# Kernel optimization log

Measured on AMD Instinct MI355X. Metric: run time of the kernel, lower is better.

## Reference

```python
import jax, jax.numpy as jnp
import numpy as np
import math

INPUT_FRAMES = 12
FUTURE_FRAMES = 26
T_STEPS = INPUT_FRAMES + FUTURE_FRAMES - 1  # 37
HD = 64   # hidden_dim
D = 16    # d_attn
CIN = 3   # input channels (time='stable')
COUT = 2  # output_dim
H, W = 24, 48


def conv2d(x, w, b, pad):
    # x: (N,C,H,W), w: (O,I,kh,kw)
    y = jax.lax.conv_general_dilated(x, w, (1, 1), [(pad, pad), (pad, pad)],
                                     dimension_numbers=('NCHW', 'OIHW', 'NCHW'))
    return y + b[None, :, None, None]


def spatial_attn(q, k, v):
    # q,k,v: (N,C,S); attention over spatial dim S
    scale = 1.0 / math.sqrt(q.shape[1])
    scores = jnp.einsum('ncs,nct->nst', q, k) * scale  # (N,S,S)
    a = jax.nn.softmax(scores, axis=-1)
    return jnp.einsum('nst,nct->ncs', a, v)


def setup_inputs() -> dict:
    key = jax.random.key(0)
    ks = jax.random.split(key, 8)
    s = 0.05
    inp = {
        'input_x': jax.random.normal(ks[0], (16, T_STEPS, H, W, CIN), dtype=jnp.float32),
        # ConvLSTM gate conv: in = CIN+HD, out = 4*HD, 3x3
        'conv_w': jax.random.normal(ks[1], (4 * HD, CIN + HD, 3, 3), dtype=jnp.float32) * s,
        'conv_b': jnp.zeros((4 * HD,), jnp.float32),
        # SA memory module
        'h_w': jax.random.normal(ks[2], (3 * D, HD, 1, 1), dtype=jnp.float32) * s,
        'h_b': jnp.zeros((3 * D,), jnp.float32),
        'm_w': jax.random.normal(ks[3], (2 * D, HD, 1, 1), dtype=jnp.float32) * s,
        'm_b': jnp.zeros((2 * D,), jnp.float32),
        'z_w': jax.random.normal(ks[4], (D, 2 * D, 1, 1), dtype=jnp.float32) * s,
        'z_b': jnp.zeros((D,), jnp.float32),
        'o_w': jax.random.normal(ks[5], (3 * HD, HD + D, 3, 3), dtype=jnp.float32) * s,
        'o_b': jnp.zeros((3 * HD,), jnp.float32),
        # final 1x1 projection to output_dim
        'out_w': jax.random.normal(ks[6], (COUT, HD, 1, 1), dtype=jnp.float32) * s,
        'out_b': jnp.zeros((COUT,), jnp.float32),
    }
    return inp


def reference(input_x, conv_w, conv_b, h_w, h_b, m_w, m_b, z_w, z_b, o_w, o_b, out_w, out_b):
    x = jnp.transpose(input_x, (0, 1, 4, 2, 3))  # (N,T,C,H,W)
    N = x.shape[0]
    S = H * W

    h0 = jnp.zeros((N, HD, H, W), x.dtype)
    carry0 = (h0, h0, h0, jnp.zeros((N, COUT, H, W), x.dtype))

    def step(carry, inp_t):
        h, c, m, prev_out = carry
        xt, t = inp_t  # xt: (N,CIN,H,W), t: scalar
        autoreg = jnp.concatenate([prev_out, xt[:, 2:]], axis=1)
        feed = jnp.where(t < INPUT_FRAMES, xt, autoreg)
        # ConvLSTM gates
        comb = conv2d(jnp.concatenate([feed, h], axis=1), conv_w, conv_b, 1)
        ci, cf, co, cg = jnp.split(comb, 4, axis=1)
        i = jax.nn.sigmoid(ci)
        f = jax.nn.sigmoid(cf)
        o = jax.nn.sigmoid(co)
        g = jnp.tanh(cg)
        c = f * c + i * g
        h = o * jnp.tanh(c)
        # self-attention memory
        hq, hk, hv = jnp.split(conv2d(h, h_w, h_b, 0), 3, axis=1)
        mk, mv = jnp.split(conv2d(m, m_w, m_b, 0), 2, axis=1)
        Zh = spatial_attn(hq.reshape(N, D, S), hk.reshape(N, D, S), hv.reshape(N, D, S))
        Zm = spatial_attn(hq.reshape(N, D, S), mk.reshape(N, D, S), mv.reshape(N, D, S))
        Z = conv2d(jnp.concatenate([Zh.reshape(N, D, H, W), Zm.reshape(N, D, H, W)], axis=1), z_w, z_b, 0)
        iog = conv2d(jnp.concatenate([Z, h], axis=1), o_w, o_b, 1)
        si, sg, so = jnp.split(iog, 3, axis=1)
        si = jax.nn.sigmoid(si)
        sg = jnp.tanh(sg)
        m = si * sg + (1.0 - si) * m
        h = jax.nn.sigmoid(so) * m
        out = conv2d(h, out_w, out_b, 0)
        return (h, c, m, out), out

    xs = (jnp.transpose(x, (1, 0, 2, 3, 4)), jnp.arange(T_STEPS))
    _, outs = jax.lax.scan(step, carry0, xs)
    outputs = jnp.transpose(outs, (1, 0, 2, 3, 4))  # (N,T,COUT,H,W)

    nino = outputs[:, -FUTURE_FRAMES:, 0, 10:13, 19:30].mean(axis=(2, 3))  # (N,26)
    nino_pred = (nino[:, :-2] + nino[:, 1:-1] + nino[:, 2:]) / 3.0          # (N,24)
    return outputs, nino_pred
```

## Files before the change

kernel.cpp:

```cpp
#include <hip/hip_runtime.h>
#include <math.h>

#define HD 64
#define DATT 16
#define NCIN 3
#define NCOUT 2
#define HH 24
#define WW 48
#define SS (HH*WW)
#define NB 16
#define TSTEPS 37
#define INPUT_FRAMES 12

#define PR 26
#define PC 52
#define PHW (PR*PC)

#define OFF_H     0
#define OFF_C     1384448
#define OFF_M     2564096
#define OFF_FEED  3743744
#define OFF_Z     3808640
#define ZERO_END  4154752
#define OFF_QKV   4154752
#define OFF_MKV   5039488
#define OFF_HB    5629312
#define OFF_IOG   8873344
#define OFF_BF2   12412288
#define OFF_BF    12596864

typedef __attribute__((ext_vector_type(8))) short short8;
typedef __attribute__((ext_vector_type(4))) float f32x4;

__device__ __forceinline__ float sigmoidf_(float x) {
    return 1.0f / (1.0f + __expf(-x));
}
__device__ __forceinline__ unsigned short f2bf(float f) {
    unsigned u = __float_as_uint(f);
    unsigned r = (u + 0x7fffu + ((u >> 16) & 1u)) >> 16;
    return (unsigned short)r;
}
__device__ __forceinline__ float bf2f(unsigned short b) {
    return __uint_as_float(((unsigned)b) << 16);
}
__device__ __forceinline__ unsigned packbf(float f) {
    unsigned short hi = f2bf(f);
    unsigned short lo = f2bf(f - bf2f(hi));
    return ((unsigned)lo << 16) | (unsigned)hi;
}
__device__ __forceinline__ float unpackbf(unsigned pk) {
    return __uint_as_float(pk << 16) + __uint_as_float(pk & 0xffff0000u);
}
__device__ __forceinline__ unsigned cvt_pk_bf16(float a, float b) {
    unsigned r;
    asm("v_cvt_pk_bf16_f32 %0, %1, %2" : "=v"(r) : "v"(a), "v"(b));
    return r;
}
__device__ __forceinline__ int permrow(int t) {
    int kb = t >> 5, tl = t & 31;
    int quad = tl >> 3, rr = tl & 7;
    return kb * 32 + ((rr >= 4) ? 16 : 0) + quad * 4 + (rr & 3);
}

__global__ void k_zero(float* __restrict__ p, int n4) {
    int i = blockIdx.x * blockDim.x + threadIdx.x;
    if (i < n4) ((float4*)p)[i] = make_float4(0.f, 0.f, 0.f, 0.f);
}

__global__ void k_prep_bf2(const float* __restrict__ cw, unsigned short* __restrict__ bbuf) {
    int idx = blockIdx.x * 256 + threadIdx.x;
    if (idx >= 344064) return;
    int j    = idx & 7;
    int lane = (idx >> 3) & 63;
    int ki   = (idx >> 9) % 21;
    int nt   = (idx / 10752) % 16;
    int p    = idx / 172032;
    int k = ki * 32 + (lane >> 4) * 8 + j;
    int ncol = nt * 16 + (lane & 15);
    unsigned short v = 0;
    if (k < 648) {
        int c = k % 72, kt = k / 72;
        if (c < 67) {
            float w = cw[ncol * 603 + c * 9 + kt];
            unsigned short hi = f2bf(w);
            v = (p == 0) ? hi : f2bf(w - bf2f(hi));
        }
    }
    bbuf[idx] = v;
}

__global__ void k_prep_bf(const float* __restrict__ ow, unsigned short* __restrict__ bbuf) {
    int idx = blockIdx.x * 256 + threadIdx.x;
    if (idx >= 282624) return;
    int j    = idx & 7;
    int lane = (idx >> 3) & 63;
    int ki   = (idx >> 9) % 23;
    int nt   = (idx / 11776) % 12;
    int p    = idx / 141312;
    int k = ki * 32 + (lane >> 4) * 8 + j;
    int ncol = nt * 16 + (lane & 15);
    unsigned short v = 0;
    if (k < 720) {
        int c = k % 80, kt = k / 80;
        float w = ow[ncol * 720 + c * 9 + kt];
        unsigned short hi = f2bf(w);
        v = (p == 0) ? hi : f2bf(w - bf2f(hi));
    }
    bbuf[idx] = v;
}

__global__ void k_feed0(const float* __restrict__ x, unsigned* __restrict__ feed) {
    int i = blockIdx.x * blockDim.x + threadIdx.x;
    if (i >= NB * 3 * SS) return;
    int s = i % SS;
    int ch = (i / SS) % 3;
    int n = i / (3 * SS);
    int y = s / WW, xx = s % WW;
    float v = x[(((size_t)(n * TSTEPS + 0) * HH + y) * WW + xx) * NCIN + ch];
    feed[((size_t)(n * 3 + ch) * PR + (y + 1)) * PC + (xx + 1)] = packbf(v);
}

#define ZOFF2 (3*52*73)
__global__ __launch_bounds__(256) void k_conv_lstm_mfma(
    const unsigned* __restrict__ feed, const unsigned* __restrict__ hin,
    const unsigned short* __restrict__ bbuf, const float* __restrict__ cb,
    float* __restrict__ c, unsigned* __restrict__ hout)
{
    __shared__ int lds[3 * 52 * 73 + 8];
    const int y0 = blockIdx.x;
    const int nb = blockIdx.y;
    const int n  = blockIdx.z;
    const int tid = threadIdx.x;

    const unsigned* fbase = feed + (size_t)n * 3 * PHW;
    const unsigned* hbase = hin + (size_t)n * HD * PHW;
    for (int e = tid; e < 11232; e += 256) {
        int cc = e / 156;
        int r2 = e - cc * 156;
        int pr = r2 / 52, pc = r2 - pr * 52;
        int v = 0;
        if (cc < 67) {
            const unsigned* src = (cc < 3) ? (fbase + (size_t)cc * PHW)
                                           : (hbase + (size_t)(cc - 3) * PHW);
            v = (int)src[(y0 + pr) * PC + pc];
        }
        lds[(pr * 52 + pc) * 73 + cc] = v;
    }
    if (tid < 8) lds[ZOFF2 + tid] = 0;
    __syncthreads();

    const int wv = tid >> 6;
    const int lane = tid & 63;
    const int mcol = lane & 15;
    const int quad = lane >> 4;

    f32x4 acc[2][3];
#pragma unroll
    for (int jg = 0; jg < 2; ++jg)
#pragma unroll
        for (int xt = 0; xt < 3; ++xt) acc[jg][xt] = (f32x4){0.f, 0.f, 0.f, 0.f};

    const unsigned short* b0 = bbuf + ((size_t)(wv * 4 + nb * 2 + 0) * 21) * 512 + lane * 8;
    const unsigned short* b1 = bbuf + ((size_t)(wv * 4 + nb * 2 + 1) * 21) * 512 + lane * 8;

    for (int ki = 0; ki < 21; ++ki) {
        short8 bh0 = *(const short8*)(b0 + ki * 512);
        short8 bl0 = *(const short8*)(b0 + ki * 512 + 172032);
        short8 bh1 = *(const short8*)(b1 + ki * 512);
        short8 bl1 = *(const short8*)(b1 + ki * 512 + 172032);

        int k0 = ki * 32 + quad * 8;
        int ab, step;
        if (k0 < 648) {
            int kt = k0 / 72;
            int c0 = k0 - kt * 72;
            int dy = kt / 3, dx = kt - dy * 3;
            ab = (dy * 52 + mcol + dx) * 73 + c0;
            step = 16 * 73;
        } else {
            ab = ZOFF2; step = 0;
        }
#pragma unroll
        for (int xt = 0; xt < 3; ++xt) {
            int abase = ab + xt * step;
            int d0 = lds[abase + 0], d1 = lds[abase + 1];
            int d2 = lds[abase + 2], d3 = lds[abase + 3];
            int d4 = lds[abase + 4], d5 = lds[abase + 5];
            int d6 = lds[abase + 6], d7 = lds[abase + 7];
            union { int i[4]; short8 v; } ah, al;
            ah.i[0] = (d1 << 16) | (d0 & 0xffff);
            ah.i[1] = (d3 << 16) | (d2 & 0xffff);
            ah.i[2] = (d5 << 16) | (d4 & 0xffff);
            ah.i[3] = (d7 << 16) | (d6 & 0xffff);
            al.i[0] = (d1 & 0xffff0000) | ((unsigned)d0 >> 16);
            al.i[1] = (d3 & 0xffff0000) | ((unsigned)d2 >> 16);
            al.i[2] = (d5 & 0xffff0000) | ((unsigned)d4 >> 16);
            al.i[3] = (d7 & 0xffff0000) | ((unsigned)d6 >> 16);

            acc[0][xt] = __builtin_amdgcn_mfma_f32_16x16x32_bf16(ah.v, bh0, acc[0][xt], 0, 0, 0);
            acc[0][xt] = __builtin_amdgcn_mfma_f32_16x16x32_bf16(ah.v, bl0, acc[0][xt], 0, 0, 0);
            acc[0][xt] = __builtin_amdgcn_mfma_f32_16x16x32_bf16(al.v, bh0, acc[0][xt], 0, 0, 0);
            acc[1][xt] = __builtin_amdgcn_mfma_f32_16x16x32_bf16(ah.v, bh1, acc[1][xt], 0, 0, 0);
            acc[1][xt] = __builtin_amdgcn_mfma_f32_16x16x32_bf16(ah.v, bl1, acc[1][xt], 0, 0, 0);
            acc[1][xt] = __builtin_amdgcn_mfma_f32_16x16x32_bf16(al.v, bh1, acc[1][xt], 0, 0, 0);
        }
    }

    __syncthreads();
    float* exch = (float*)lds;
#pragma unroll
    for (int jg = 0; jg < 2; ++jg)
#pragma unroll
        for (int xt = 0; xt < 3; ++xt)
#pragma unroll
            for (int r = 0; r < 4; ++r)
                exch[((wv * 2 + jg) * 3 + xt) * 272 + (quad * 4 + r) * 17 + mcol] = acc[jg][xt][r];
    __syncthreads();

    const int ch32 = tid & 31;
    const int xg = tid >> 5;
    const int jg = ch32 >> 4, col = ch32 & 15;
    const int gch = nb * 32 + ch32;
    const float bi = cb[gch], bfv = cb[64 + gch], bo = cb[128 + gch], bg = cb[192 + gch];
    size_t cbase = ((size_t)(n * HD + gch) * HH + y0) * WW;
    unsigned* hp = hout + ((size_t)(n * HD + gch) * PR + y0 + 1) * PC + 1;
#pragma unroll
    for (int k = 0; k < 6; ++k) {
        int x = xg * 6 + k;
        int xt = x >> 4, row = x & 15;
        float iv = sigmoidf_(exch[((0 * 2 + jg) * 3 + xt) * 272 + row * 17 + col] + bi);
        float fv = sigmoidf_(exch[((1 * 2 + jg) * 3 + xt) * 272 + row * 17 + col] + bfv);
        float ov = sigmoidf_(exch[((2 * 2 + jg) * 3 + xt) * 272 + row * 17 + col] + bo);
        float gv = tanhf    (exch[((3 * 2 + jg) * 3 + xt) * 272 + row * 17 + col] + bg);
        float cold = c[cbase + x];
        float cn = fv * cold + iv * gv;
        float hn = ov * tanhf(cn);
        c[cbase + x] = cn;
        hp[x] = packbf(hn);
    }
}

#define ZOFF (3*52*81)
__global__ __launch_bounds__(192) void k_conv_mfma(
    const unsigned* __restrict__ Zin, const unsigned* __restrict__ hin,
    const unsigned short* __restrict__ bbuf, const float* __restrict__ ob,
    float* __restrict__ iog)
{
    __shared__ int lds[3 * 52 * 81 + 8];
    const int y0 = blockIdx.x;
    const int nb = blockIdx.y;
    const int n  = blockIdx.z;
    const int tid = threadIdx.x;

    const unsigned* zbase = Zin + (size_t)n * DATT * PHW;
    const unsigned* hbase = hin + (size_t)n * HD * PHW;
    for (int e = tid; e < 12480; e += 192) {
        int cc = e / 156;
        int r2 = e - cc * 156;
        int pr = r2 / 52, pc = r2 - pr * 52;
        const unsigned* src = (cc < 16) ? (zbase + (size_t)cc * PHW)
                                        : (hbase + (size_t)(cc - 16) * PHW);
        lds[(pr * 52 + pc) * 81 + cc] = (int)src[(y0 + pr) * PC + pc];
    }
    if (tid < 8) lds[ZOFF + tid] = 0;
    __syncthreads();

    const int wv = tid >> 6;
    const int lane = tid & 63;
    const int mcol = lane & 15;
    const int quad = lane >> 4;

    f32x4 acc[2][3];
#pragma unroll
    for (int j = 0; j < 2; ++j)
#pragma unroll
        for (int xt = 0; xt < 3; ++xt) acc[j][xt] = (f32x4){0.f, 0.f, 0.f, 0.f};

    const unsigned short* bb = bbuf + (size_t)(nb * 6) * 23 * 512;
    const unsigned short* b0 = bb + ((size_t)(wv * 2 + 0) * 23) * 512 + lane * 8;
    const unsigned short* b1 = bb + ((size_t)(wv * 2 + 1) * 23) * 512 + lane * 8;

    for (int ki = 0; ki < 23; ++ki) {
        short8 bh0 = *(const short8*)(b0 + ki * 512);
        short8 bl0 = *(const short8*)(b0 + ki * 512 + 141312);
        short8 bh1 = *(const short8*)(b1 + ki * 512);
        short8 bl1 = *(const short8*)(b1 + ki * 512 + 141312);

        int k0 = ki * 32 + quad * 8;
        int ab, step;
        if (k0 < 720) {
            int kt = k0 / 80;
            int c0 = k0 - kt * 80;
            int dy = kt / 3, dx = kt - dy * 3;
            ab = (dy * 52 + mcol + dx) * 81 + c0;
            step = 16 * 81;
        } else {
            ab = ZOFF; step = 0;
        }
#pragma unroll
        for (int xt = 0; xt < 3; ++xt) {
            int abase = ab + xt * step;
            int d0 = lds[abase + 0], d1 = lds[abase + 1];
            int d2 = lds[abase + 2], d3 = lds[abase + 3];
            int d4 = lds[abase + 4], d5 = lds[abase + 5];
            int d6 = lds[abase + 6], d7 = lds[abase + 7];
            union { int i[4]; short8 v; } ah, al;
            ah.i[0] = (d1 << 16) | (d0 & 0xffff);
            ah.i[1] = (d3 << 16) | (d2 & 0xffff);
            ah.i[2] = (d5 << 16) | (d4 & 0xffff);
            ah.i[3] = (d7 << 16) | (d6 & 0xffff);
            al.i[0] = (d1 & 0xffff0000) | ((unsigned)d0 >> 16);
            al.i[1] = (d3 & 0xffff0000) | ((unsigned)d2 >> 16);
            al.i[2] = (d5 & 0xffff0000) | ((unsigned)d4 >> 16);
            al.i[3] = (d7 & 0xffff0000) | ((unsigned)d6 >> 16);

            acc[0][xt] = __builtin_amdgcn_mfma_f32_16x16x32_bf16(ah.v, bh0, acc[0][xt], 0, 0, 0);
            acc[0][xt] = __builtin_amdgcn_mfma_f32_16x16x32_bf16(ah.v, bl0, acc[0][xt], 0, 0, 0);
            acc[0][xt] = __builtin_amdgcn_mfma_f32_16x16x32_bf16(al.v, bh0, acc[0][xt], 0, 0, 0);
            acc[1][xt] = __builtin_amdgcn_mfma_f32_16x16x32_bf16(ah.v, bh1, acc[1][xt], 0, 0, 0);
            acc[1][xt] = __builtin_amdgcn_mfma_f32_16x16x32_bf16(ah.v, bl1, acc[1][xt], 0, 0, 0);
            acc[1][xt] = __builtin_amdgcn_mfma_f32_16x16x32_bf16(al.v, bh1, acc[1][xt], 0, 0, 0);
        }
    }

#pragma unroll
    for (int j = 0; j < 2; ++j) {
        int oc = nb * 96 + (wv * 2 + j) * 16 + mcol;
        float bv = ob[oc];
#pragma unroll
        for (int xt = 0; xt < 3; ++xt) {
            int sbase = y0 * 48 + xt * 16 + quad * 4;
            float* dst = iog + ((size_t)n * 192 + oc) * 1152 + sbase;
#pragma unroll
            for (int r = 0; r < 4; ++r) dst[r] = acc[j][xt][r] + bv;
        }
    }
}

__global__ __launch_bounds__(256) void k_qkv(
    const unsigned* __restrict__ h, const float* __restrict__ m,
    const float* __restrict__ hw, const float* __restrict__ hb,
    const float* __restrict__ mw, const float* __restrict__ mb,
    unsigned short* __restrict__ pl) {
    __shared__ float lw[512];
    __shared__ float lb[8];
    const int g = blockIdx.y;
    const int tid = threadIdx.x;
    const float* wsrc = (g < 6) ? (hw + g * 512) : (mw + (g - 6) * 512);
    const float* bsrc = (g < 6) ? (hb + g * 8) : (mb + (g - 6) * 8);
    for (int i = tid; i < 512; i += 256) lw[i] = wsrc[i];
    if (tid < 8) lb[tid] = bsrc[tid];
    __syncthreads();

    int idx = blockIdx.x * 256 + tid;
    int s = idx % SS;
    int n = idx / SS;

    float reg[HD];
    if (g < 6) {
        int y = s / WW, x = s % WW;
        const unsigned* src = h + (size_t)n * HD * PHW + (y + 1) * PC + (x + 1);
#pragma unroll
        for (int ic = 0; ic < HD; ++ic) reg[ic] = unpackbf(src[ic * PHW]);
    } else {
        const float* src = m + (size_t)n * HD * SS + s;
#pragma unroll
        for (int ic = 0; ic < HD; ++ic) reg[ic] = src[ic * SS];
    }

    float out[8];
#pragma unroll
    for (int j = 0; j < 8; ++j) {
        const float* wr = &lw[j * HD];
        float a = lb[j];
#pragma unroll
        for (int ic = 0; ic < HD; ++ic) a += reg[ic] * wr[ic];
        out[j] = a;
    }

    unsigned short* bq  = pl;
    unsigned short* akh = pl + 294912;
    unsigned short* akm = pl + 589824;
    unsigned short* bvh = pl + 884736;
    unsigned short* bvm = pl + 1179648;
    const int c0 = (g & 1) * 8;

    if (g < 2) {
        unsigned w0 = (unsigned)f2bf(out[0]) | ((unsigned)f2bf(out[1]) << 16);
        unsigned w1 = (unsigned)f2bf(out[2]) | ((unsigned)f2bf(out[3]) << 16);
        unsigned w2 = (unsigned)f2bf(out[4]) | ((unsigned)f2bf(out[5]) << 16);
        unsigned w3 = (unsigned)f2bf(out[6]) | ((unsigned)f2bf(out[7]) << 16);
        *(uint4*)&bq[((size_t)n * SS + s) * 16 + c0] = make_uint4(w0, w1, w2, w3);
    } else if (g < 4 || (g >= 6 && g < 8)) {
        int row = permrow(s);
        unsigned short* base = (g < 4) ? akh : akm;
        unsigned w0 = (unsigned)f2bf(out[0]) | ((unsigned)f2bf(out[1]) << 16);
        unsigned w1 = (unsigned)f2bf(out[2]) | ((unsigned)f2bf(out[3]) << 16);
        unsigned w2 = (unsigned)f2bf(out[4]) | ((unsigned)f2bf(out[5]) << 16);
        unsigned w3 = (unsigned)f2bf(out[6]) | ((unsigned)f2bf(out[7]) << 16);
        *(uint4*)&base[((size_t)n * SS + row) * 16 + c0] = make_uint4(w0, w1, w2, w3);
    } else {
        unsigned short* base = (g < 6) ? bvh : bvm;
#pragma unroll
        for (int j = 0; j < 8; ++j)
            base[((size_t)n * 16 + c0 + j) * SS + s] = f2bf(out[j]);
    }
}

__global__ __launch_bounds__(256) void k_attn(
    const unsigned short* __restrict__ pl, const unsigned short* __restrict__ zbuf,
    const float* __restrict__ zw, const float* __restrict__ zb,
    unsigned* __restrict__ Z)
{
    __shared__ float ldsO[4][2][16][16];
    __shared__ float ldsF[2][16][16];
    __shared__ float ldsL[4][2][16];
    __shared__ float ldsLF[2][16];

    const int n   = blockIdx.x;
    const int qt  = blockIdx.y;
    const int tid = threadIdx.x;
    const int wv  = tid >> 6;
    const int lane = tid & 63;
    const int col  = lane & 15;
    const int quad = lane >> 4;
    const bool hi  = quad >= 2;

    const unsigned short* bq  = pl;
    const unsigned short* akh = pl + 294912;
    const unsigned short* akm = pl + 589824;
    const unsigned short* bvh = pl + 884736;
    const unsigned short* bvm = pl + 1179648;

    const size_t nb = (size_t)n * 18432;
    const int stepk = hi ? 0 : 512;
    const int subk  = hi ? 0 : 256;
    const unsigned short* qp  = hi ? zbuf : (bq  + nb + ((size_t)(qt * 16 + col)) * 16 + quad * 8);
    const unsigned short* khb = hi ? zbuf : (akh + nb + col * 16 + quad * 8);
    const unsigned short* kmb = hi ? zbuf : (akm + nb + col * 16 + quad * 8);
    const unsigned short* vhb = bvh + nb + (size_t)col * SS + quad * 8;
    const unsigned short* vmb = bvm + nb + (size_t)col * SS + quad * 8;

    short8 qf = *(const short8*)qp;

    f32x4 oh = (f32x4){0.f,0.f,0.f,0.f}, om = (f32x4){0.f,0.f,0.f,0.f};
    float lh = 0.f, lm = 0.f;
    const int kb0 = wv * 9, kb1 = kb0 + 9;
    for (int kb = kb0; kb < kb1; ++kb) {
        const unsigned short* kh0 = khb + (size_t)kb * stepk;
        const unsigned short* km0 = kmb + (size_t)kb * stepk;
        short8 khA = *(const short8*)kh0;
        short8 khB = *(const short8*)(kh0 + subk);
        short8 kmA = *(const short8*)km0;
        short8 kmB = *(const short8*)(km0 + subk);
        short8 vh  = *(const short8*)(vhb + (size_t)kb * 32);
        short8 vm  = *(const short8*)(vmb + (size_t)kb * 32);
        const f32x4 z4 = (f32x4){0.f,0.f,0.f,0.f};
        f32x4 sA = __builtin_amdgcn_mfma_f32_16x16x32_bf16(khA, qf, z4, 0, 0, 0);
        f32x4 sB = __builtin_amdgcn_mfma_f32_16x16x32_bf16(khB, qf, z4, 0, 0, 0);
        f32x4 tA = __builtin_amdgcn_mfma_f32_16x16x32_bf16(kmA, qf, z4, 0, 0, 0);
        f32x4 tB = __builtin_amdgcn_mfma_f32_16x16x32_bf16(kmB, qf, z4, 0, 0, 0);

        float pa0 = __expf(0.25f * sA[0]), pa1 = __expf(0.25f * sA[1]);
        float pa2 = __expf(0.25f * sA[2]), pa3 = __expf(0.25f * sA[3]);
        float pb0 = __expf(0.25f * sB[0]), pb1 = __expf(0.25f * sB[1]);
        float pb2 = __expf(0.25f * sB[2]), pb3 = __expf(0.25f * sB[3]);
        lh += (pa0 + pa1 + pa2 + pa3) + (pb0 + pb1 + pb2 + pb3);
        union { unsigned u[4]; short8 v; } ph;
        ph.u[0] = cvt_pk_bf16(pa0, pa1); ph.u[1] = cvt_pk_bf16(pa2, pa3);
        ph.u[2] = cvt_pk_bf16(pb0, pb1); ph.u[3] = cvt_pk_bf16(pb2, pb3);
        oh = __builtin_amdgcn_mfma_f32_16x16x32_bf16(ph.v, vh, oh, 0, 0, 0);

        float qa0 = __expf(0.25f * tA[0]), qa1 = __expf(0.25f * tA[1]);
        float qa2 = __expf(0.25f * tA[2]), qa3 = __expf(0.25f * tA[3]);
        float qb0 = __expf(0.25f * tB[0]), qb1 = __expf(0.25f * tB[1]);
        float qb2 = __expf(0.25f * tB[2]), qb3 = __expf(0.25f * tB[3]);
        lm += (qa0 + qa1 + qa2 + qa3) + (qb0 + qb1 + qb2 + qb3);
        union { unsigned u[4]; short8 v; } pm;
        pm.u[0] = cvt_pk_bf16(qa0, qa1); pm.u[1] = cvt_pk_bf16(qa2, qa3);
        pm.u[2] = cvt_pk_bf16(qb0, qb1); pm.u[3] = cvt_pk_bf16(qb2, qb3);
        om = __builtin_amdgcn_mfma_f32_16x16x32_bf16(pm.v, vm, om, 0, 0, 0);
    }

    lh += __shfl_xor(lh, 16); lh += __shfl_xor(lh, 32);
    lm += __shfl_xor(lm, 16); lm += __shfl_xor(lm, 32);

#pragma unroll
    for (int r = 0; r < 4; ++r) {
        ldsO[wv][0][quad * 4 + r][col] = oh[r];
        ldsO[wv][1][quad * 4 + r][col] = om[r];
    }
    if (lane < 16) { ldsL[wv][0][lane] = lh; ldsL[wv][1][lane] = lm; }
    __syncthreads();

    if (tid < 128) {
        int a_ = tid >> 6, rem = tid & 63, q_ = rem >> 2, j4 = (rem & 3) * 4;
        float4 s4 = make_float4(0.f, 0.f, 0.f, 0.f);
#pragma unroll
        for (int w = 0; w < 4; ++w) {
            float4 v = *(const float4*)&ldsO[w][a_][q_][j4];
            s4.x += v.x; s4.y += v.y; s4.z += v.z; s4.w += v.w;
        }
        *(float4*)&ldsF[a_][q_][j4] = s4;
    } else if (tid < 160) {
        int e = tid - 128, a_ = e >> 4, q_ = e & 15;
        ldsLF[a_][q_] = ldsL[0][a_][q_] + ldsL[1][a_][q_] +
                        ldsL[2][a_][q_] + ldsL[3][a_][q_];
    }
    __syncthreads();

    const int q  = tid & 15;
    const int zc = tid >> 4;
    float iLh = 1.f / ldsLF[0][q], iLm = 1.f / ldsLF[1][q];
    const float* zr = zw + zc * 32;
    float a = zb[zc];
#pragma unroll
    for (int j = 0; j < 16; ++j)
        a += zr[j] * (ldsF[0][q][j] * iLh) + zr[16 + j] * (ldsF[1][q][j] * iLm);
    int s = qt * 16 + q;
    int y = s / WW, x = s % WW;
    Z[((size_t)(n * DATT + zc) * PR + y + 1) * PC + x + 1] = packbf(a);
}

__global__ void k_sa_gates(const float* __restrict__ iog, float* __restrict__ m,
                           unsigned* __restrict__ h) {
    int i = blockIdx.x * blockDim.x + threadIdx.x;
    if (i >= NB * HD * SS) return;
    int s = i % SS;
    int ch = (i / SS) % HD;
    int n = i / (HD * SS);
    const float* ib = iog + (size_t)n * 3 * HD * SS;
    float si = ib[ch * SS + s];
    float sg = ib[(HD + ch) * SS + s];
    float so = ib[(2 * HD + ch) * SS + s];
    si = sigmoidf_(si);
    sg = tanhf(sg);
    float mn = si * sg + (1.f - si) * m[i];
    m[i] = mn;
    int y = s / WW, x = s % WW;
    h[((size_t)(n * HD + ch) * PR + (y + 1)) * PC + (x + 1)] = packbf(sigmoidf_(so) * mn);
}

__global__ void k_out_feed(const unsigned* __restrict__ h, const float* __restrict__ ow,
                           const float* __restrict__ ob, const float* __restrict__ x,
                           float* __restrict__ outbuf, unsigned* __restrict__ feed, int t) {
    int idx = blockIdx.x * 256 + threadIdx.x;
    if (idx >= NB * SS) return;
    int s = idx % SS;
    int n = idx / SS;
    int y = s / WW, xx = s % WW;
    const unsigned* src = h + (size_t)n * HD * PHW + (y + 1) * PC + (xx + 1);
    float o0 = ob[0], o1 = ob[1];
#pragma unroll
    for (int ic = 0; ic < HD; ++ic) {
        float r = unpackbf(src[ic * PHW]);
        o0 += r * ow[ic];
        o1 += r * ow[HD + ic];
    }
    outbuf[(((size_t)n * TSTEPS + t) * NCOUT + 0) * SS + s] = o0;
    outbuf[(((size_t)n * TSTEPS + t) * NCOUT + 1) * SS + s] = o1;

    if (t + 1 < TSTEPS) {
        int t1 = t + 1;
        const float* xp = &x[(((size_t)(n * TSTEPS + t1) * HH + y) * WW + xx) * NCIN];
        float f0, f1, f2 = xp[2];
        if (t1 < INPUT_FRAMES) { f0 = xp[0]; f1 = xp[1]; }
        else { f0 = o0; f1 = o1; }
        size_t fb = ((size_t)(n * 3 + 0) * PR + y + 1) * PC + xx + 1;
        feed[fb] = packbf(f0);
        feed[fb + PHW] = packbf(f1);
        feed[fb + 2 * (size_t)PHW] = packbf(f2);
    }
}

__global__ void k_nino(const float* __restrict__ outbuf, float* __restrict__ pred) {
    int tidx = threadIdx.x;
    if (tidx >= 16 * 24) return;
    int j = tidx % 24;
    int n = tidx / 24;
    float acc = 0.f;
    for (int f = j; f < j + 3; ++f) {
        int t = 11 + f;
        const float* p = &outbuf[(((size_t)n * TSTEPS + t) * NCOUT + 0) * SS];
        float sloc = 0.f;
        for (int y = 10; y <= 12; ++y)
            for (int x = 19; x <= 29; ++x)
                sloc += p[y * WW + x];
        acc += sloc * (1.f / 33.f);
    }
    pred[n * 24 + j] = acc * (1.f / 3.f);
}

extern "C" void kernel_launch(void* const* d_in, const int* in_sizes, int n_in,
                              void* d_out, int out_size, void* d_ws, size_t ws_size,
                              hipStream_t stream) {
    const float* x      = (const float*)d_in[0];
    const float* conv_w = (const float*)d_in[1];
    const float* conv_b = (const float*)d_in[2];
    const float* h_w    = (const float*)d_in[3];
    const float* h_b    = (const float*)d_in[4];
    const float* m_w    = (const float*)d_in[5];
    const float* m_b    = (const float*)d_in[6];
    const float* z_w    = (const float*)d_in[7];
    const float* z_b    = (const float*)d_in[8];
    const float* o_w    = (const float*)d_in[9];
    const float* o_b    = (const float*)d_in[10];
    const float* out_w  = (const float*)d_in[11];
    const float* out_b  = (const float*)d_in[12];

    float* ws   = (float*)d_ws;
    unsigned* hA   = (unsigned*)(ws + OFF_H);
    float* c    = ws + OFF_C;
    float* m    = ws + OFF_M;
    unsigned* feedp = (unsigned*)(ws + OFF_FEED);
    unsigned* Zp    = (unsigned*)(ws + OFF_Z);
    unsigned* hB    = (unsigned*)(ws + OFF_HB);
    float* iog  = ws + OFF_IOG;
    unsigned short* bf2 = (unsigned short*)(ws + OFF_BF2);
    unsigned short* bf  = (unsigned short*)(ws + OFF_BF);
    unsigned short* planes = (unsigned short*)(ws + OFF_QKV);
    const unsigned short* zbuf = (const unsigned short*)(ws + OFF_MKV);
    float* outp = (float*)d_out;

    k_zero<<<4058, 256, 0, stream>>>(ws, 1038688);
    k_zero<<<1352, 256, 0, stream>>>(ws + OFF_HB, 346112);
    k_zero<<<1, 64, 0, stream>>>(ws + OFF_MKV, 16);
    k_prep_bf2<<<1344, 256, 0, stream>>>(conv_w, bf2);
    k_prep_bf<<<1104, 256, 0, stream>>>(o_w, bf);
    k_feed0<<<216, 256, 0, stream>>>(x, feedp);

    for (int t = 0; t < TSTEPS; ++t) {
        k_conv_lstm_mfma<<<dim3(24, 2, 16), 256, 0, stream>>>(feedp, hB, bf2, conv_b, c, hA);
        k_qkv<<<dim3(72, 10), 256, 0, stream>>>(hA, m, h_w, h_b, m_w, m_b, planes);
        k_attn<<<dim3(16, 72), 256, 0, stream>>>(planes, zbuf, z_w, z_b, Zp);
        k_conv_mfma<<<dim3(24, 2, 16), 192, 0, stream>>>(Zp, hA, bf, o_b, iog);
        k_sa_gates<<<4608, 256, 0, stream>>>(iog, m, hB);
        k_out_feed<<<72, 256, 0, stream>>>(hB, out_w, out_b, x, outp, feedp, t);
    }
    k_nino<<<1, 384, 0, stream>>>(outp, outp + (size_t)NB * TSTEPS * NCOUT * SS);
}
```

Before: 4.251 ms.

## Fuse SA gate epilogue into output conv, vectorize LDS loads, prefetch weights

Merges the SA-memory gate elementwise kernel into the o_w conv kernel. Output channels are regrouped per block so each block holds matching si/sg/so gates for 32 channels, and the block updates m and h directly, which removes the iog round-trip through global memory and one launch per step. Both MFMA conv kernels now pad LDS rows to a multiple of 4 ints so staging and A-fragment reads can use int4 accesses. They also software-prefetch the next K-slice of B weights into registers. The changes add register pressure and alter the LDS bank pattern through the new strides.

```diff
diff --git a/kernel.cpp b/kernel.cpp
--- a/kernel.cpp
+++ b/kernel.cpp
@@ -61,6 +61,17 @@
     int quad = tl >> 3, rr = tl & 7;
     return kb * 32 + ((rr >= 4) ? 16 : 0) + quad * 4 + (rr & 3);
 }
+
+#define MKFRAG(P0, P1, ah, al) do {                                  \
+    ah.i[0] = (P0.y << 16) | (P0.x & 0xffff);                        \
+    ah.i[1] = (P0.w << 16) | (P0.z & 0xffff);                        \
+    ah.i[2] = (P1.y << 16) | (P1.x & 0xffff);                        \
+    ah.i[3] = (P1.w << 16) | (P1.z & 0xffff);                        \
+    al.i[0] = (P0.y & 0xffff0000) | ((unsigned)P0.x >> 16);          \
+    al.i[1] = (P0.w & 0xffff0000) | ((unsigned)P0.z >> 16);          \
+    al.i[2] = (P1.y & 0xffff0000) | ((unsigned)P1.x >> 16);          \
+    al.i[3] = (P1.w & 0xffff0000) | ((unsigned)P1.z >> 16);          \
+} while (0)
 
 __global__ void k_zero(float* __restrict__ p, int n4) {
     int i = blockIdx.x * blockDim.x + threadIdx.x;
@@ -120,13 +131,14 @@
     feed[((size_t)(n * 3 + ch) * PR + (y + 1)) * PC + (xx + 1)] = packbf(v);
 }
 
-#define ZOFF2 (3*52*73)
+#define ASTR2 76
+#define ZOFF2 (3*52*ASTR2)
 __global__ __launch_bounds__(256) void k_conv_lstm_mfma(
     const unsigned* __restrict__ feed, const unsigned* __restrict__ hin,
     const unsigned short* __restrict__ bbuf, const float* __restrict__ cb,
     float* __restrict__ c, unsigned* __restrict__ hout)
 {
-    __shared__ int lds[3 * 52 * 73 + 8];
+    __shared__ __align__(16) int lds[3 * 52 * ASTR2 + 8];
     const int y0 = blockIdx.x;
     const int nb = blockIdx.y;
     const int n  = blockIdx.z;
@@ -134,17 +146,22 @@
 
     const unsigned* fbase = feed + (size_t)n * 3 * PHW;
     const unsigned* hbase = hin + (size_t)n * HD * PHW;
-    for (int e = tid; e < 11232; e += 256) {
-        int cc = e / 156;
-        int r2 = e - cc * 156;
+    for (int e = tid; e < 2808; e += 256) {
+        int grp = e / 156;
+        int r2  = e - grp * 156;
         int pr = r2 / 52, pc = r2 - pr * 52;
-        int v = 0;
-        if (cc < 67) {
-            const unsigned* src = (cc < 3) ? (fbase + (size_t)cc * PHW)
-                                           : (hbase + (size_t)(cc - 3) * PHW);
-            v = (int)src[(y0 + pr) * PC + pc];
+        int cc0 = grp * 4;
+        int vv[4];
+#pragma unroll
+        for (int j = 0; j < 4; ++j) {
+            int cc = cc0 + j;
+            int t = 0;
+            if (cc < 3)        t = (int)fbase[(size_t)cc * PHW + (y0 + pr) * PC + pc];
+            else if (cc < 67)  t = (int)hbase[(size_t)(cc - 3) * PHW + (y0 + pr) * PC + pc];
+            vv[j] = t;
         }
-        lds[(pr * 52 + pc) * 73 + cc] = v;
+        int4 v; v.x = vv[0]; v.y = vv[1]; v.z = vv[2]; v.w = vv[3];
+        *(int4*)&lds[r2 * ASTR2 + cc0] = v;
     }
     if (tid < 8) lds[ZOFF2 + tid] = 0;
     __syncthreads();
@@ -163,11 +180,17 @@
     const unsigned short* b0 = bbuf + ((size_t)(wv * 4 + nb * 2 + 0) * 21) * 512 + lane * 8;
     const unsigned short* b1 = bbuf + ((size_t)(wv * 4 + nb * 2 + 1) * 21) * 512 + lane * 8;
 
+    short8 cb0h = *(const short8*)(b0);
+    short8 cb0l = *(const short8*)(b0 + 172032);
+    short8 cb1h = *(const short8*)(b1);
+    short8 cb1l = *(const short8*)(b1 + 172032);
+
     for (int ki = 0; ki < 21; ++ki) {
-        short8 bh0 = *(const short8*)(b0 + ki * 512);
-        short8 bl0 = *(const short8*)(b0 + ki * 512 + 172032);
-        short8 bh1 = *(const short8*)(b1 + ki * 512);
-        short8 bl1 = *(const short8*)(b1 + ki * 512 + 172032);
+        int kn = (ki < 20) ? (ki + 1) * 512 : 20 * 512;
+        short8 nb0h = *(const short8*)(b0 + kn);
+        short8 nb0l = *(const short8*)(b0 + kn + 172032);
+        short8 nb1h = *(const short8*)(b1 + kn);
+        short8 nb1l = *(const short8*)(b1 + kn + 172032);
 
         int k0 = ki * 32 + quad * 8;
         int ab, step;
@@ -175,35 +198,39 @@
             int kt = k0 / 72;
             int c0 = k0 - kt * 72;
             int dy = kt / 3, dx = kt - dy * 3;
-            ab = (dy * 52 + mcol + dx) * 73 + c0;
-            step = 16 * 73;
+            ab = (dy * 52 + mcol + dx) * ASTR2 + c0;
+            step = 16 * ASTR2;
         } else {
             ab = ZOFF2; step = 0;
         }
-#pragma unroll
-        for (int xt = 0; xt < 3; ++xt) {
-            int abase = ab + xt * step;
-            int d0 = lds[abase + 0], d1 = lds[abase + 1];
-            int d2 = lds[abase + 2], d3 = lds[abase + 3];
-            int d4 = lds[abase + 4], d5 = lds[abase + 5];
-            int d6 = lds[abase + 6], d7 = lds[abase + 7];
-            union { int i[4]; short8 v; } ah, al;
-            ah.i[0] = (d1 << 16) | (d0 & 0xffff);
-            ah.i[1] = (d3 << 16) | (d2 & 0xffff);
-            ah.i[2] = (d5 << 16) | (d4 & 0xffff);
-            ah.i[3] = (d7 << 16) | (d6 & 0xffff);
-            al.i[0] = (d1 & 0xffff0000) | ((unsigned)d0 >> 16);
-            al.i[1] = (d3 & 0xffff0000) | ((unsigned)d2 >> 16);
-            al.i[2] = (d5 & 0xffff0000) | ((unsigned)d4 >> 16);
-            al.i[3] = (d7 & 0xffff0000) | ((unsigned)d6 >> 16);
-
-            acc[0][xt] = __builtin_amdgcn_mfma_f32_16x16x32_bf16(ah.v, bh0, acc[0][xt], 0, 0, 0);
-            acc[0][xt] = __builtin_amdgcn_mfma_f32_16x16x32_bf16(ah.v, bl0, acc[0][xt], 0, 0, 0);
-            acc[0][xt] = __builtin_amdgcn_mfma_f32_16x16x32_bf16(al.v, bh0, acc[0][xt], 0, 0, 0);
-            acc[1][xt] = __builtin_amdgcn_mfma_f32_16x16x32_bf16(ah.v, bh1, acc[1][xt], 0, 0, 0);
-            acc[1][xt] = __builtin_amdgcn_mfma_f32_16x16x32_bf16(ah.v, bl1, acc[1][xt], 0, 0, 0);
-            acc[1][xt] = __builtin_amdgcn_mfma_f32_16x16x32_bf16(al.v, bh1, acc[1][xt], 0, 0, 0);
-        }
+        int4 A0 = *(const int4*)&lds[ab],            A1 = *(const int4*)&lds[ab + 4];
+        int4 B0 = *(const int4*)&lds[ab + step],     B1 = *(const int4*)&lds[ab + step + 4];
+        int4 C0 = *(const int4*)&lds[ab + 2 * step], C1 = *(const int4*)&lds[ab + 2 * step + 4];
+
+        union { int i[4]; short8 v; } ah, al;
+        MKFRAG(A0, A1, ah, al);
+        acc[0][0] = __builtin_amdgcn_mfma_f32_16x16x32_bf16(ah.v, cb0h, acc[0][0], 0, 0, 0);
+        acc[0][0] = __builtin_amdgcn_mfma_f32_16x16x32_bf16(ah.v, cb0l, acc[0][0], 0, 0, 0);
+        acc[0][0] = __builtin_amdgcn_mfma_f32_16x16x32_bf16(al.v, cb0h, acc[0][0], 0, 0, 0);
+        acc[1][0] = __builtin_amdgcn_mfma_f32_16x16x32_bf16(ah.v, cb1h, acc[1][0], 0, 0, 0);
+        acc[1][0] = __builtin_amdgcn_mfma_f32_16x16x32_bf16(ah.v, cb1l, acc[1][0], 0, 0, 0);
+        acc[1][0] = __builtin_amdgcn_mfma_f32_16x16x32_bf16(al.v, cb1h, acc[1][0], 0, 0, 0);
+        MKFRAG(B0, B1, ah, al);
+        acc[0][1] = __builtin_amdgcn_mfma_f32_16x16x32_bf16(ah.v, cb0h, acc[0][1], 0, 0, 0);
+        acc[0][1] = __builtin_amdgcn_mfma_f32_16x16x32_bf16(ah.v, cb0l, acc[0][1], 0, 0, 0);
+        acc[0][1] = __builtin_amdgcn_mfma_f32_16x16x32_bf16(al.v, cb0h, acc[0][1], 0, 0, 0);
+        acc[1][1] = __builtin_amdgcn_mfma_f32_16x16x32_bf16(ah.v, cb1h, acc[1][1], 0, 0, 0);
+        acc[1][1] = __builtin_amdgcn_mfma_f32_16x16x32_bf16(ah.v, cb1l, acc[1][1], 0, 0, 0);
+        acc[1][1] = __builtin_amdgcn_mfma_f32_16x16x32_bf16(al.v, cb1h, acc[1][1], 0, 0, 0);
+        MKFRAG(C0, C1, ah, al);
+        acc[0][2] = __builtin_amdgcn_mfma_f32_16x16x32_bf16(ah.v, cb0h, acc[0][2], 0, 0, 0);
+        acc[0][2] = __builtin_amdgcn_mfma_f32_16x16x32_bf16(ah.v, cb0l, acc[0][2], 0, 0, 0);
+        acc[0][2] = __builtin_amdgcn_mfma_f32_16x16x32_bf16(al.v, cb0h, acc[0][2], 0, 0, 0);
+        acc[1][2] = __builtin_amdgcn_mfma_f32_16x16x32_bf16(ah.v, cb1h, acc[1][2], 0, 0, 0);
+        acc[1][2] = __builtin_amdgcn_mfma_f32_16x16x32_bf16(ah.v, cb1l, acc[1][2], 0, 0, 0);
+        acc[1][2] = __builtin_amdgcn_mfma_f32_16x16x32_bf16(al.v, cb1h, acc[1][2], 0, 0, 0);
+
+        cb0h = nb0h; cb0l = nb0l; cb1h = nb1h; cb1l = nb1l;
     }
 
     __syncthreads();
@@ -240,27 +267,36 @@
     }
 }
 
-#define ZOFF (3*52*81)
-__global__ __launch_bounds__(192) void k_conv_mfma(
+#define ASTR (84)
+#define ZOFF (3*52*ASTR)
+__global__ __launch_bounds__(192) void k_conv_sa(
     const unsigned* __restrict__ Zin, const unsigned* __restrict__ hin,
     const unsigned short* __restrict__ bbuf, const float* __restrict__ ob,
-    float* __restrict__ iog)
+    float* __restrict__ m, unsigned* __restrict__ hout)
 {
-    __shared__ int lds[3 * 52 * 81 + 8];
+    __shared__ __align__(16) int lds[3 * 52 * ASTR + 8];
     const int y0 = blockIdx.x;
-    const int nb = blockIdx.y;
+    const int cbk = blockIdx.y;
     const int n  = blockIdx.z;
     const int tid = threadIdx.x;
 
     const unsigned* zbase = Zin + (size_t)n * DATT * PHW;
     const unsigned* hbase = hin + (size_t)n * HD * PHW;
-    for (int e = tid; e < 12480; e += 192) {
-        int cc = e / 156;
-        int r2 = e - cc * 156;
+    for (int e = tid; e < 3120; e += 192) {
+        int grp = e / 156;
+        int r2  = e - grp * 156;
         int pr = r2 / 52, pc = r2 - pr * 52;
-        const unsigned* src = (cc < 16) ? (zbase + (size_t)cc * PHW)
-                                        : (hbase + (size_t)(cc - 16) * PHW);
-        lds[(pr * 52 + pc) * 81 + cc] = (int)src[(y0 + pr) * PC + pc];
+        int cc0 = grp * 4;
+        int vv[4];
+#pragma unroll
+        for (int j = 0; j < 4; ++j) {
+            int cc = cc0 + j;
+            const unsigned* src = (cc < 16) ? (zbase + (size_t)cc * PHW)
+                                            : (hbase + (size_t)(cc - 16) * PHW);
+            vv[j] = (int)src[(y0 + pr) * PC + pc];
+        }
+        int4 v; v.x = vv[0]; v.y = vv[1]; v.z = vv[2]; v.w = vv[3];
+        *(int4*)&lds[r2 * ASTR + cc0] = v;
     }
     if (tid < 8) lds[ZOFF + tid] = 0;
     __syncthreads();
@@ -276,15 +312,20 @@
 #pragma unroll
         for (int xt = 0; xt < 3; ++xt) acc[j][xt] = (f32x4){0.f, 0.f, 0.f, 0.f};
 
-    const unsigned short* bb = bbuf + (size_t)(nb * 6) * 23 * 512;
-    const unsigned short* b0 = bb + ((size_t)(wv * 2 + 0) * 23) * 512 + lane * 8;
-    const unsigned short* b1 = bb + ((size_t)(wv * 2 + 1) * 23) * 512 + lane * 8;
+    const unsigned short* b0 = bbuf + ((size_t)(wv * 4 + cbk * 2 + 0) * 23) * 512 + lane * 8;
+    const unsigned short* b1 = bbuf + ((size_t)(wv * 4 + cbk * 2 + 1) * 23) * 512 + lane * 8;
+
+    short8 cb0h = *(const short8*)(b0);
+    short8 cb0l = *(const short8*)(b0 + 141312);
+    short8 cb1h = *(const short8*)(b1);
+    short8 cb1l = *(const short8*)(b1 + 141312);
 
     for (int ki = 0; ki < 23; ++ki) {
-        short8 bh0 = *(const short8*)(b0 + ki * 512);
-        short8 bl0 = *(const short8*)(b0 + ki * 512 + 141312);
-        short8 bh1 = *(const short8*)(b1 + ki * 512);
-        short8 bl1 = *(const short8*)(b1 + ki * 512 + 141312);
+        int kn = (ki < 22) ? (ki + 1) * 512 : 22 * 512;
+        short8 nb0h = *(const short8*)(b0 + kn);
+        short8 nb0l = *(const short8*)(b0 + kn + 141312);
+        short8 nb1h = *(const short8*)(b1 + kn);
+        short8 nb1l = *(const short8*)(b1 + kn + 141312);
 
         int k0 = ki * 32 + quad * 8;
         int ab, step;
@@ -292,48 +333,70 @@
             int kt = k0 / 80;
             int c0 = k0 - kt * 80;
             int dy = kt / 3, dx = kt - dy * 3;
-            ab = (dy * 52 + mcol + dx) * 81 + c0;
-            step = 16 * 81;
+            ab = (dy * 52 + mcol + dx) * ASTR + c0;
+            step = 16 * ASTR;
         } else {
             ab = ZOFF; step = 0;
         }
-#pragma unroll
-        for (int xt = 0; xt < 3; ++xt) {
-            int abase = ab + xt * step;
-            int d0 = lds[abase + 0], d1 = lds[abase + 1];
-            int d2 = lds[abase + 2], d3 = lds[abase + 3];
-            int d4 = lds[abase + 4], d5 = lds[abase + 5];
-            int d6 = lds[abase + 6], d7 = lds[abase + 7];
-            union { int i[4]; short8 v; } ah, al;
-            ah.i[0] = (d1 << 16) | (d0 & 0xffff);
-            ah.i[1] = (d3 << 16) | (d2 & 0xffff);
-            ah.i[2] = (d5 << 16) | (d4 & 0xffff);
-            ah.i[3] = (d7 << 16) | (d6 & 0xffff);
-            al.i[0] = (d1 & 0xffff0000) | ((unsigned)d0 >> 16);
-            al.i[1] = (d3 & 0xffff0000) | ((unsigned)d2 >> 16);
-            al.i[2] = (d5 & 0xffff0000) | ((unsigned)d4 >> 16);
-            al.i[3] = (d7 & 0xffff0000) | ((unsigned)d6 >> 16);
-
-            acc[0][xt] = __builtin_amdgcn_mfma_f32_16x16x32_bf16(ah.v, bh0, acc[0][xt], 0, 0, 0);
-            acc[0][xt] = __builtin_amdgcn_mfma_f32_16x16x32_bf16(ah.v, bl0, acc[0][xt], 0, 0, 0);
-            acc[0][xt] = __builtin_amdgcn_mfma_f32_16x16x32_bf16(al.v, bh0, acc[0][xt], 0, 0, 0);
-            acc[1][xt] = __builtin_amdgcn_mfma_f32_16x16x32_bf16(ah.v, bh1, acc[1][xt], 0, 0, 0);
-            acc[1][xt] = __builtin_amdgcn_mfma_f32_16x16x32_bf16(ah.v, bl1, acc[1][xt], 0, 0, 0);
-            acc[1][xt] = __builtin_amdgcn_mfma_f32_16x16x32_bf16(al.v, bh1, acc[1][xt], 0, 0, 0);
-        }
-    }
-
-#pragma unroll
-    for (int j = 0; j < 2; ++j) {
-        int oc = nb * 96 + (wv * 2 + j) * 16 + mcol;
-        float bv = ob[oc];
-#pragma unroll
-        for (int xt = 0; xt < 3; ++xt) {
-            int sbase = y0 * 48 + xt * 16 + quad * 4;
-            float* dst = iog + ((size_t)n * 192 + oc) * 1152 + sbase;
-#pragma unroll
-            for (int r = 0; r < 4; ++r) dst[r] = acc[j][xt][r] + bv;
-        }
+        int4 A0 = *(const int4*)&lds[ab],            A1 = *(const int4*)&lds[ab + 4];
+        int4 B0 = *(const int4*)&lds[ab + step],     B1 = *(const int4*)&lds[ab + step + 4];
+        int4 C0 = *(const int4*)&lds[ab + 2 * step], C1 = *(const int4*)&lds[ab + 2 * step + 4];
+
+        union { int i[4]; short8 v; } ah, al;
+        MKFRAG(A0, A1, ah, al);
+        acc[0][0] = __builtin_amdgcn_mfma_f32_16x16x32_bf16(ah.v, cb0h, acc[0][0], 0, 0, 0);
+        acc[0][0] = __builtin_amdgcn_mfma_f32_16x16x32_bf16(ah.v, cb0l, acc[0][0], 0, 0, 0);
+        acc[0][0] = __builtin_amdgcn_mfma_f32_16x16x32_bf16(al.v, cb0h, acc[0][0], 0, 0, 0);
+        acc[1][0] = __builtin_amdgcn_mfma_f32_16x16x32_bf16(ah.v, cb1h, acc[1][0], 0, 0, 0);
+        acc[1][0] = __builtin_amdgcn_mfma_f32_16x16x32_bf16(ah.v, cb1l, acc[1][0], 0, 0, 0);
+        acc[1][0] = __builtin_amdgcn_mfma_f32_16x16x32_bf16(al.v, cb1h, acc[1][0], 0, 0, 0);
+        MKFRAG(B0, B1, ah, al);
+        acc[0][1] = __builtin_amdgcn_mfma_f32_16x16x32_bf16(ah.v, cb0h, acc[0][1], 0, 0, 0);
+        acc[0][1] = __builtin_amdgcn_mfma_f32_16x16x32_bf16(ah.v, cb0l, acc[0][1], 0, 0, 0);
+        acc[0][1] = __builtin_amdgcn_mfma_f32_16x16x32_bf16(al.v, cb0h, acc[0][1], 0, 0, 0);
+        acc[1][1] = __builtin_amdgcn_mfma_f32_16x16x32_bf16(ah.v, cb1h, acc[1][1], 0, 0, 0);
+        acc[1][1] = __builtin_amdgcn_mfma_f32_16x16x32_bf16(ah.v, cb1l, acc[1][1], 0, 0, 0);
+        acc[1][1] = __builtin_amdgcn_mfma_f32_16x16x32_bf16(al.v, cb1h, acc[1][1], 0, 0, 0);
+        MKFRAG(C0, C1, ah, al);
+        acc[0][2] = __builtin_amdgcn_mfma_f32_16x16x32_bf16(ah.v, cb0h, acc[0][2], 0, 0, 0);
+        acc[0][2] = __builtin_amdgcn_mfma_f32_16x16x32_bf16(ah.v, cb0l, acc[0][2], 0, 0, 0);
+        acc[0][2] = __builtin_amdgcn_mfma_f32_16x16x32_bf16(al.v, cb0h, acc[0][2], 0, 0, 0);
+        acc[1][2] = __builtin_amdgcn_mfma_f32_16x16x32_bf16(ah.v, cb1h, acc[1][2], 0, 0, 0);
+        acc[1][2] = __builtin_amdgcn_mfma_f32_16x16x32_bf16(ah.v, cb1l, acc[1][2], 0, 0, 0);
+        acc[1][2] = __builtin_amdgcn_mfma_f32_16x16x32_bf16(al.v, cb1h, acc[1][2], 0, 0, 0);
+
+        cb0h = nb0h; cb0l = nb0l; cb1h = nb1h; cb1l = nb1l;
+    }
+
+    __syncthreads();
+    float* exch = (float*)lds;
+#pragma unroll
+    for (int j = 0; j < 2; ++j)
+#pragma unroll
+        for (int xt = 0; xt < 3; ++xt)
+#pragma unroll
+            for (int r = 0; r < 4; ++r)
+                exch[((wv * 2 + j) * 3 + xt) * 272 + (quad * 4 + r) * 17 + mcol] = acc[j][xt][r];
+    __syncthreads();
+
+    const int ch32 = tid & 31;
+    const int xg = tid >> 5;
+    const int jg = ch32 >> 4, col = ch32 & 15;
+    const int gch = cbk * 32 + ch32;
+    const float bsi = ob[gch], bsg = ob[64 + gch], bso = ob[128 + gch];
+    float* mrow = m + ((size_t)(n * HD + gch) * HH + y0) * WW;
+    unsigned* hp = hout + ((size_t)(n * HD + gch) * PR + y0 + 1) * PC + 1;
+#pragma unroll
+    for (int k = 0; k < 8; ++k) {
+        int x = xg * 8 + k;
+        int xt = x >> 4, row = x & 15;
+        float si = sigmoidf_(exch[((0 * 2 + jg) * 3 + xt) * 272 + row * 17 + col] + bsi);
+        float sg = tanhf    (exch[((1 * 2 + jg) * 3 + xt) * 272 + row * 17 + col] + bsg);
+        float so =           exch[((2 * 2 + jg) * 3 + xt) * 272 + row * 17 + col] + bso;
+        float mo = mrow[x];
+        float mn = si * sg + (1.f - si) * mo;
+        mrow[x] = mn;
+        hp[x] = packbf(sigmoidf_(so) * mn);
     }
 }
 
@@ -522,25 +585,6 @@
     Z[((size_t)(n * DATT + zc) * PR + y + 1) * PC + x + 1] = packbf(a);
 }
 
-__global__ void k_sa_gates(const float* __restrict__ iog, float* __restrict__ m,
-                           unsigned* __restrict__ h) {
-    int i = blockIdx.x * blockDim.x + threadIdx.x;
-    if (i >= NB * HD * SS) return;
-    int s = i % SS;
-    int ch = (i / SS) % HD;
-    int n = i / (HD * SS);
-    const float* ib = iog + (size_t)n * 3 * HD * SS;
-    float si = ib[ch * SS + s];
-    float sg = ib[(HD + ch) * SS + s];
-    float so = ib[(2 * HD + ch) * SS + s];
-    si = sigmoidf_(si);
-    sg = tanhf(sg);
-    float mn = si * sg + (1.f - si) * m[i];
-    m[i] = mn;
-    int y = s / WW, x = s % WW;
-    h[((size_t)(n * HD + ch) * PR + (y + 1)) * PC + (x + 1)] = packbf(sigmoidf_(so) * mn);
-}
-
 __global__ void k_out_feed(const unsigned* __restrict__ h, const float* __restrict__ ow,
                            const float* __restrict__ ob, const float* __restrict__ x,
                            float* __restrict__ outbuf, unsigned* __restrict__ feed, int t) {
@@ -609,13 +653,12 @@
     const float* out_b  = (const float*)d_in[12];
 
     float* ws   = (float*)d_ws;
-    unsigned* hA   = (unsigned*)(ws + OFF_H);
+    unsigned* hA    = (unsigned*)(ws + OFF_H);
     float* c    = ws + OFF_C;
     float* m    = ws + OFF_M;
     unsigned* feedp = (unsigned*)(ws + OFF_FEED);
     unsigned* Zp    = (unsigned*)(ws + OFF_Z);
     unsigned* hB    = (unsigned*)(ws + OFF_HB);
-    float* iog  = ws + OFF_IOG;
     unsigned short* bf2 = (unsigned short*)(ws + OFF_BF2);
     unsigned short* bf  = (unsigned short*)(ws + OFF_BF);
     unsigned short* planes = (unsigned short*)(ws + OFF_QKV);
@@ -633,8 +676,7 @@
         k_conv_lstm_mfma<<<dim3(24, 2, 16), 256, 0, stream>>>(feedp, hB, bf2, conv_b, c, hA);
         k_qkv<<<dim3(72, 10), 256, 0, stream>>>(hA, m, h_w, h_b, m_w, m_b, planes);
         k_attn<<<dim3(16, 72), 256, 0, stream>>>(planes, zbuf, z_w, z_b, Zp);
-        k_conv_mfma<<<dim3(24, 2, 16), 192, 0, stream>>>(Zp, hA, bf, o_b, iog);
-        k_sa_gates<<<4608, 256, 0, stream>>>(iog, m, hB);
+        k_conv_sa<<<dim3(24, 2, 16), 192, 0, stream>>>(Zp, hA, bf, o_b, m, hB);
         k_out_feed<<<72, 256, 0, stream>>>(hB, out_w, out_b, x, outp, feedp, t);
     }
     k_nino<<<1, 384, 0, stream>>>(outp, outp + (size_t)NB * TSTEPS * NCOUT * SS);
```

Measured after the change: 3.915 ms. -7.9%, faster.
